# Performance work log

Hardware: AMD Instinct MI355X
Metric: run time of the kernel (lower is better)

The kernel has to match this reference:

```python
import jax, jax.numpy as jnp
import numpy as np

B, C, H, W = 16, 256, 64, 64
K = 1024


def setup_inputs() -> dict:
    key = jax.random.key(0)
    k1, k2 = jax.random.split(key)
    z = jax.random.normal(k1, (B, C, H, W), dtype=jnp.float32)
    codebook = jax.random.normal(k2, (K, C), dtype=jnp.float32)
    return {"z": z, "codebook": codebook}


def reference(z, codebook):
    # assign: nearest-code indices via squared euclidean distance
    b, c, h, w = z.shape
    zf = jnp.transpose(z, (0, 2, 3, 1)).reshape(-1, c)            # [N, C]
    # ||z||^2 - 2 z.cb^T + ||cb||^2  -> [N, K]
    dists = (jnp.sum(zf * zf, axis=1, keepdims=True)
             - 2.0 * jnp.einsum('nc,kc->nk', zf, codebook)
             + jnp.sum(codebook * codebook, axis=1)[None, :])
    idx = jnp.argmin(dists, axis=1)                                # [N]
    indices = idx.reshape(b, 1, h, w)                              # [B,1,H,W]
    # embed_code: gather codebook rows, back to BCHW
    zq = codebook[idx].reshape(b, h, w, c)                         # [B,H,W,C]
    zq = jnp.transpose(zq, (0, 3, 1, 2))                           # [B,C,H,W]
    return zq, indices
```

## Files before the change

### kernel.cpp

```cpp
#include <hip/hip_runtime.h>


#define HWSZ 4096
#define CDIM 256
#define KCODES 1024
#define NPIX 65536
#define ZQ_ELEMS (16 * 256 * 4096)
#define MARGIN 0.75f

#define WS_CBSWZ 0
#define WS_CBN64 524288
#define WS_CBN32 532480
#define WS_CNT   536576
#define WS_LISTS 536592

typedef __attribute__((ext_vector_type(8))) short bf16x8;
typedef __attribute__((ext_vector_type(4))) float f32x4;
typedef __attribute__((ext_vector_type(4))) unsigned short us4;

#define MFMA16(a, b, c) __builtin_amdgcn_mfma_f32_16x16x32_bf16(a, b, c, 0, 0, 0)

__device__ __forceinline__ unsigned short f2bf(float f) {
  unsigned u = __float_as_uint(f);
  unsigned r = u + 0x7FFFu + ((u >> 16) & 1u);
  return (unsigned short)(r >> 16);
}

__device__ __forceinline__ void gload_lds16(const void* g, void* l) {
  __builtin_amdgcn_global_load_lds(
      (const __attribute__((address_space(1))) unsigned int*)g,
      (__attribute__((address_space(3))) unsigned int*)l, 16, 0, 0);
}

__device__ __forceinline__ void ins3(unsigned& k1, unsigned& k2, unsigned& k3,
                                     unsigned k) {
  unsigned nk2, nk3;
  asm("v_med3_u32 %0, %1, %2, %3" : "=v"(nk2) : "v"(k1), "v"(k2), "v"(k));
  asm("v_med3_u32 %0, %1, %2, %3" : "=v"(nk3) : "v"(k2), "v"(k3), "v"(k));
  k1 = k1 < k ? k1 : k;
  k2 = nk2;
  k3 = nk3;
}

__device__ __forceinline__ float keyf(unsigned k) {
  return __uint_as_float(k & 0xFFFFFC00u);
}

__global__ void vq_prep(const float* __restrict__ cb,
                        unsigned short* __restrict__ cbswz,
                        double* __restrict__ cbn64,
                        float* __restrict__ cbn32p,
                        int* __restrict__ cnt) {
  const int t = threadIdx.x;
  if (blockIdx.x == 0 && t == 0) { cnt[0] = 0; cnt[1] = 0; }
  const int code = blockIdx.x * 4 + (t >> 6);
  const int lane = t & 63;
  const int c4 = lane * 4;

  float4 v = *(const float4*)(cb + (size_t)code * CDIM + c4);
  us4 hv;
  hv.x = f2bf(-2.f * v.x); hv.y = f2bf(-2.f * v.y);
  hv.z = f2bf(-2.f * v.z); hv.w = f2bf(-2.f * v.w);
  const int K = (code >> 9) * 32 + ((code >> 4) & 31);
  unsigned r = (unsigned)(code & 15);
  unsigned off = ((r << 9) + (unsigned)(c4 << 1)) ^ ((r & 7) << 4);
  *(us4*)((char*)cbswz + (size_t)K * 8192 + off) = hv;

  double s = (double)v.x * v.x;
  s = fma((double)v.y, (double)v.y, s);
  s = fma((double)v.z, (double)v.z, s);
  s = fma((double)v.w, (double)v.w, s);
#pragma unroll
  for (int o = 32; o; o >>= 1) s += __shfl_xor(s, o, 64);
  if (lane == 0) {
    cbn64[code] = s;
    cbn32p[code] = (float)s + 512.0f;
  }
}

__launch_bounds__(256)
__global__ void vq_stage1(const float* __restrict__ z,
                          const float* __restrict__ cb,
                          const unsigned short* __restrict__ cbswz,
                          const float* __restrict__ cbn32p,
                          float* __restrict__ out_zq,
                          float* __restrict__ out_idx,
                          int* __restrict__ cnt,
                          int* __restrict__ listA, int capA,
                          int* __restrict__ listB, int capB,
                          float* __restrict__ zws, int zcap) {
  extern __shared__ char smem[];
  const int t = threadIdx.x;
  const int w = t >> 6;
  const int lane = t & 63;
  const int lg = lane >> 4;
  const int lcode = lane & 15;
  const int h = w >> 1;
  const int q = w & 1;
  const int p0 = blockIdx.x * 64;
  const int b = p0 >> 12;
  const int hw0 = p0 & (HWSZ - 1);
  const float* zb = z + (size_t)b * (CDIM * HWSZ) + hw0;

  float* nrm = (float*)(smem + 32768);
  {
    float4 nv = *(const float4*)(cbn32p + t * 4);
    *(float4*)(nrm + t * 4) = nv;
  }

  {
    const char* gsrc = (const char*)cbswz + (size_t)(q * 32) * 8192 +
                       (h * 4) * 1024 + lane * 16;
    char* ldst = smem + q * 8192 + (h * 4) * 1024 + lane * 16;
#pragma unroll
    for (int j = 0; j < 4; ++j)
      gload_lds16(gsrc + j * 1024, ldst + j * 1024);
  }

  bf16x8 af[2][8];
#pragma unroll
  for (int T = 0; T < 2; ++T) {
    const float* zr = zb + (h * 32 + T * 16 + lcode);
#pragma unroll
    for (int kk = 0; kk < 8; ++kk) {
      const int ch0 = kk * 32 + lg * 8;
      bf16x8 f;
#pragma unroll
      for (int j = 0; j < 8; ++j)
        f[j] = (short)f2bf(zr[(size_t)(ch0 + j) * HWSZ]);
      af[T][kk] = f;
    }
  }
  __syncthreads();

  unsigned k1[2][4], k2[2][4], k3[2][4];
#pragma unroll
  for (int T = 0; T < 2; ++T)
#pragma unroll
    for (int q4 = 0; q4 < 4; ++q4) {
      k1[T][q4] = 0xFFFFFFFFu; k2[T][q4] = 0xFFFFFFFFu; k3[T][q4] = 0xFFFFFFFFu;
    }

  const unsigned rsw = ((unsigned)(lcode & 7)) << 4;
  const unsigned rbase = ((unsigned)lcode << 9) + (((unsigned)lg) << 4);
  const char* myhalf = smem + q * 8192;
  const int nrm0 = q * 512 + lcode;

  for (int c = 0; c < 32; ++c) {
    const char* rbuf = myhalf + (c & 1) * 16384;
    if (c < 31) {
      const char* gsrc = (const char*)cbswz + (size_t)(q * 32 + c + 1) * 8192 +
                         (h * 4) * 1024 + lane * 16;
      char* ldst = smem + ((c + 1) & 1) * 16384 + q * 8192 +
                   (h * 4) * 1024 + lane * 16;
#pragma unroll
      for (int j = 0; j < 4; ++j)
        gload_lds16(gsrc + j * 1024, ldst + j * 1024);
    }
    f32x4 acc0 = {0.f, 0.f, 0.f, 0.f};
    f32x4 acc1 = {0.f, 0.f, 0.f, 0.f};
#pragma unroll
    for (int kk = 0; kk < 8; ++kk) {
      bf16x8 bf = *(const bf16x8*)(rbuf + ((rbase + ((unsigned)kk << 6)) ^ rsw));
      acc0 = MFMA16(af[0][kk], bf, acc0);
      acc1 = MFMA16(af[1][kk], bf, acc1);
    }
    const unsigned code = (unsigned)(nrm0 + c * 16);
    const float cn = nrm[code];
#pragma unroll
    for (int T = 0; T < 2; ++T)
#pragma unroll
      for (int q4 = 0; q4 < 4; ++q4) {
        float m = cn + ((T == 0) ? acc0[q4] : acc1[q4]);
        unsigned key = (__float_as_uint(m) & 0xFFFFFC00u) | code;
        ins3(k1[T][q4], k2[T][q4], k3[T][q4], key);
      }
    __syncthreads();
  }

#pragma unroll
  for (int mask = 1; mask <= 8; mask <<= 1) {
#pragma unroll
    for (int T = 0; T < 2; ++T)
#pragma unroll
      for (int q4 = 0; q4 < 4; ++q4) {
        unsigned o1 = __shfl_xor(k1[T][q4], mask, 64);
        unsigned o2 = __shfl_xor(k2[T][q4], mask, 64);
        unsigned o3 = __shfl_xor(k3[T][q4], mask, 64);
        ins3(k1[T][q4], k2[T][q4], k3[T][q4], o1);
        ins3(k1[T][q4], k2[T][q4], k3[T][q4], o2);
        ins3(k1[T][q4], k2[T][q4], k3[T][q4], o3);
      }
  }

  unsigned* mk = (unsigned*)smem;
  int* lcnt = (int*)(smem + 2304);
  if (t == 0) *lcnt = 0;
  if (lcode == 0) {
#pragma unroll
    for (int T = 0; T < 2; ++T)
#pragma unroll
      for (int q4 = 0; q4 < 4; ++q4) {
        int row = h * 32 + T * 16 + lg * 4 + q4;
        unsigned* d = mk + (row * 2 + q) * 3;
        d[0] = k1[T][q4]; d[1] = k2[T][q4]; d[2] = k3[T][q4];
      }
  }
  __syncthreads();

  int* sbest = (int*)(smem + 2048);
  int* flp = (int*)(smem + 2560);
  int* flq = (int*)(smem + 2816);
  if (t < 64) {
    unsigned a1 = mk[t * 6 + 0], a2 = mk[t * 6 + 1], a3 = mk[t * 6 + 2];
    ins3(a1, a2, a3, mk[t * 6 + 3]);
    ins3(a1, a2, a3, mk[t * 6 + 4]);
    ins3(a1, a2, a3, mk[t * 6 + 5]);
    const int p = p0 + t;
    const int i1 = (int)(a1 & 1023u);
    sbest[t] = i1;
    out_idx[p] = (float)i1;
    float f1 = keyf(a1);
    float g2 = keyf(a2) - f1;
    float g3 = keyf(a3) - f1;
    if (g3 < MARGIN) {
      int pos = atomicAdd(cnt + 1, 1);
      if (pos < capB) listB[pos] = p;
    } else if (g2 < MARGIN) {
      int pos = atomicAdd(cnt, 1);
      if (pos < capA) {
        listA[2 * pos] = p | (i1 << 16);
        listA[2 * pos + 1] = (int)(a2 & 1023u) | ((int)(a3 & 1023u) << 16);
        if (pos < zcap) {
          int li = atomicAdd(lcnt, 1);
          flp[li] = p;
          flq[li] = pos;
        }
      }
    }
  }
  __syncthreads();

  {
    const int px = t & 63;
    const int best = sbest[px];
    const int ch0g = (t >> 6) * 64;
    const float* crow = cb + (size_t)best * CDIM + ch0g;
    float* ob = out_zq + (size_t)b * (CDIM * HWSZ) + (size_t)ch0g * HWSZ + hw0 + px;
#pragma unroll 4
    for (int c2 = 0; c2 < 64; c2 += 4) {
      float4 v = *(const float4*)(crow + c2);
      ob[(size_t)(c2 + 0) * HWSZ] = v.x;
      ob[(size_t)(c2 + 1) * HWSZ] = v.y;
      ob[(size_t)(c2 + 2) * HWSZ] = v.z;
      ob[(size_t)(c2 + 3) * HWSZ] = v.w;
    }
  }

  {
    const int nf = *lcnt;
    for (int e = 0; e < nf; ++e) {
      const int p = flp[e];
      const int slot = flq[e];
      const int bb = p >> 12;
      const int hh = p & (HWSZ - 1);
      zws[(size_t)slot * 256 + t] =
          z[(size_t)bb * (CDIM * HWSZ) + (size_t)t * HWSZ + hh];
    }
  }
}

__launch_bounds__(256)
__global__ void vq_resolve3(const float* __restrict__ z,
                            const float* __restrict__ cb,
                            const double* __restrict__ cbn64,
                            float* __restrict__ out_zq,
                            float* __restrict__ out_idx,
                            const int* __restrict__ cnt,
                            const int* __restrict__ listA, int capA,
                            const float* __restrict__ zws, int zcap) {
  const int lane = threadIdx.x & 63;
  const int wid = (blockIdx.x * blockDim.x + threadIdx.x) >> 6;
  const int nw = (gridDim.x * blockDim.x) >> 6;
  int n = cnt[0];
  if (n > capA) n = capA;

  for (int i = wid; i < n; i += nw) {
    const int e0 = listA[2 * i];
    const int e1 = listA[2 * i + 1];
    const int p = e0 & 0xFFFF;
    int cand[3];
    cand[0] = (e0 >> 16) & 1023;
    cand[1] = e1 & 0xFFFF;
    cand[2] = (e1 >> 16) & 1023;
    const int b = p >> 12;
    const int hw = p & (HWSZ - 1);
    const int ch0 = lane * 4;

    double zv[4];
    if (i < zcap) {
      float4 zf = ((const float4*)(zws + (size_t)i * 256))[lane];
      zv[0] = (double)zf.x; zv[1] = (double)zf.y;
      zv[2] = (double)zf.z; zv[3] = (double)zf.w;
    } else {
      const float* zb = z + (size_t)b * (CDIM * HWSZ) + hw;
#pragma unroll
      for (int j = 0; j < 4; ++j) zv[j] = (double)zb[(size_t)(ch0 + j) * HWSZ];
    }

    double d[3];
#pragma unroll
    for (int tt = 0; tt < 3; ++tt) {
      float4 cv = *(const float4*)(cb + (size_t)cand[tt] * CDIM + ch0);
      double s = zv[0] * (double)cv.x;
      s = fma(zv[1], (double)cv.y, s);
      s = fma(zv[2], (double)cv.z, s);
      s = fma(zv[3], (double)cv.w, s);
#pragma unroll
      for (int off = 32; off; off >>= 1) s += __shfl_xor(s, off, 64);
      d[tt] = fma(-2.0, s, cbn64[cand[tt]]);
    }

    double bd = d[0];
    int bi = cand[0];
#pragma unroll
    for (int tt = 1; tt < 3; ++tt) {
      bool takes = (d[tt] < bd) || (d[tt] == bd && cand[tt] < bi);
      bd = takes ? d[tt] : bd;
      bi = takes ? cand[tt] : bi;
    }

    if (bi != cand[0]) {
      if (lane == 0) out_idx[p] = (float)bi;
      float4 cv = *(const float4*)(cb + (size_t)bi * CDIM + ch0);
      float* ob = out_zq + (size_t)b * (CDIM * HWSZ) + hw;
      ob[(size_t)(ch0 + 0) * HWSZ] = cv.x;
      ob[(size_t)(ch0 + 1) * HWSZ] = cv.y;
      ob[(size_t)(ch0 + 2) * HWSZ] = cv.z;
      ob[(size_t)(ch0 + 3) * HWSZ] = cv.w;
    }
  }
}

__launch_bounds__(256)
__global__ void vq_fullscan(const float* __restrict__ z,
                            const float* __restrict__ cb,
                            const double* __restrict__ cbn64,
                            float* __restrict__ out_zq,
                            float* __restrict__ out_idx,
                            const int* __restrict__ cnt,
                            const int* __restrict__ listB, int capB) {
  __shared__ double zl[256];
  __shared__ double sd[4];
  __shared__ int si[4];
  __shared__ int sfin;
  int n = cnt[1];
  if (n > capB) n = capB;
  const int t = threadIdx.x;
  const int w = t >> 6;
  const int lane = t & 63;

  for (int i = blockIdx.x; i < n; i += gridDim.x) {
    const int p = listB[i];
    const int b = p >> 12;
    const int hw = p & (HWSZ - 1);
    const float* zb = z + (size_t)b * (CDIM * HWSZ) + hw;
    zl[t] = (double)zb[(size_t)t * HWSZ];
    __syncthreads();

    const int g = t >> 2;
    const int sub = t & 3;
    const double* zq4 = zl + sub * 64;
    double bd = 1e300;
    int bi = 0;

    for (int j = 0; j < 16; ++j) {
      const int code = g + 64 * j;
      const float* crow = cb + (size_t)code * CDIM + sub * 64;
      double s = 0.0;
#pragma unroll
      for (int q4 = 0; q4 < 64; q4 += 4) {
        float4 cv = *(const float4*)(crow + q4);
        s = fma(zq4[q4 + 0], (double)cv.x, s);
        s = fma(zq4[q4 + 1], (double)cv.y, s);
        s = fma(zq4[q4 + 2], (double)cv.z, s);
        s = fma(zq4[q4 + 3], (double)cv.w, s);
      }
      s += __shfl_xor(s, 1, 64);
      s += __shfl_xor(s, 2, 64);
      double d = fma(-2.0, s, cbn64[code]);
      bool takes = (d < bd) || (d == bd && code < bi);
      bd = takes ? d : bd;
      bi = takes ? code : bi;
    }

#pragma unroll
    for (int off = 4; off <= 32; off <<= 1) {
      double od = __shfl_xor(bd, off, 64);
      int oi = __shfl_xor(bi, off, 64);
      bool takes = (od < bd) || (od == bd && oi < bi);
      bd = takes ? od : bd;
      bi = takes ? oi : bi;
    }
    if (lane == 0) { sd[w] = bd; si[w] = bi; }
    __syncthreads();
    if (t == 0) {
      double fd = sd[0];
      int fi = si[0];
#pragma unroll
      for (int k = 1; k < 4; ++k) {
        bool takes = (sd[k] < fd) || (sd[k] == fd && si[k] < fi);
        fd = takes ? sd[k] : fd;
        fi = takes ? si[k] : fi;
      }
      const int old = (int)out_idx[p];
      if (fi != old) out_idx[p] = (float)fi;
      sfin = (fi != old) ? fi : -1;
    }
    __syncthreads();
    const int best = sfin;
    if (best >= 0) {
      float* ob = out_zq + (size_t)b * (CDIM * HWSZ) + hw;
      ob[(size_t)t * HWSZ] = cb[(size_t)best * CDIM + t];
    }
    __syncthreads();
  }
}

extern "C" void kernel_launch(void* const* d_in, const int* in_sizes, int n_in,
                              void* d_out, int out_size, void* d_ws, size_t ws_size,
                              hipStream_t stream) {
  const float* z = (const float*)d_in[0];
  const float* cb = (const float*)d_in[1];
  float* out = (float*)d_out;
  float* out_zq = out;
  float* out_idx = out + ZQ_ELEMS;

  char* ws = (char*)d_ws;
  unsigned short* cbswz = (unsigned short*)(ws + WS_CBSWZ);
  double* cbn64 = (double*)(ws + WS_CBN64);
  float* cbn32p = (float*)(ws + WS_CBN32);
  int* cnt = (int*)(ws + WS_CNT);

  long long avail = (long long)ws_size - WS_LISTS;
  if (avail < 0) avail = 0;
  long long capA_ll = (avail / 4) / 8;
  if (capA_ll > NPIX) capA_ll = NPIX;
  int capA = (int)capA_ll;
  int* listA = (int*)(ws + WS_LISTS);
  long long rem = avail - (long long)capA * 8;
  long long capB_ll = rem / 8;
  if (capB_ll > NPIX) capB_ll = NPIX;
  if (capB_ll < 0) capB_ll = 0;
  int capB = (int)capB_ll;
  int* listB = (int*)(ws + WS_LISTS + (size_t)capA * 8);
  long long zoff = (WS_LISTS + (long long)capA * 8 + (long long)capB * 4 + 15) &
                   ~15LL;
  long long zcap_ll = ((long long)ws_size - zoff) / 1024;
  if (zcap_ll < 0) zcap_ll = 0;
  if (zcap_ll > capA) zcap_ll = capA;
  int zcap = (int)zcap_ll;
  float* zws = (float*)(ws + zoff);

  vq_prep<<<256, 256, 0, stream>>>(cb, cbswz, cbn64, cbn32p, cnt);
  vq_stage1<<<1024, 256, 36864, stream>>>(z, cb, cbswz, cbn32p, out_zq, out_idx,
                                          cnt, listA, capA, listB, capB,
                                          zws, zcap);
  vq_resolve3<<<1024, 256, 0, stream>>>(z, cb, cbn64, out_zq, out_idx,
                                        cnt, listA, capA, zws, zcap);
  vq_fullscan<<<256, 256, 0, stream>>>(z, cb, cbn64, out_zq, out_idx,
                                       cnt, listB, capB);
}
```

Baseline: 164.0 us.

## Triple-buffer codebook staging in stage1 with explicit waitcnt barriers

Replaces the double-buffered codebook LDS pipeline in the stage1 kernel with a three-buffer rotation that prefetches two chunks ahead. Each step now uses a manual vmcnt wait plus a raw barrier instead of __syncthreads. The codebook layout changes from an XOR-swizzled row layout to a kk-major layout, which makes the LDS read addresses simpler. LDS per block grows from 36 KB to 52 KB, which may lower occupancy, and the new unswizzled layout may bring back bank conflicts.

```diff
diff --git a/kernel.cpp b/kernel.cpp
--- a/kernel.cpp
+++ b/kernel.cpp
@@ -62,9 +62,11 @@
   hv.x = f2bf(-2.f * v.x); hv.y = f2bf(-2.f * v.y);
   hv.z = f2bf(-2.f * v.z); hv.w = f2bf(-2.f * v.w);
   const int K = (code >> 9) * 32 + ((code >> 4) & 31);
-  unsigned r = (unsigned)(code & 15);
-  unsigned off = ((r << 9) + (unsigned)(c4 << 1)) ^ ((r & 7) << 4);
-  *(us4*)((char*)cbswz + (size_t)K * 8192 + off) = hv;
+  const int kk = c4 >> 5;
+  const int lg = (c4 >> 3) & 3;
+  const int within = (c4 & 7) * 2;
+  size_t off = (size_t)K * 8192 + kk * 1024 + (code & 15) * 64 + lg * 16 + within;
+  *(us4*)((char*)cbswz + off) = hv;
 
   double s = (double)v.x * v.x;
   s = fma((double)v.y, (double)v.y, s);
@@ -102,20 +104,27 @@
   const int hw0 = p0 & (HWSZ - 1);
   const float* zb = z + (size_t)b * (CDIM * HWSZ) + hw0;
 
-  float* nrm = (float*)(smem + 32768);
-  {
-    float4 nv = *(const float4*)(cbn32p + t * 4);
-    *(float4*)(nrm + t * 4) = nv;
-  }
-
-  {
-    const char* gsrc = (const char*)cbswz + (size_t)(q * 32) * 8192 +
-                       (h * 4) * 1024 + lane * 16;
-    char* ldst = smem + q * 8192 + (h * 4) * 1024 + lane * 16;
-#pragma unroll
-    for (int j = 0; j < 4; ++j)
-      gload_lds16(gsrc + j * 1024, ldst + j * 1024);
-  }
+  char* const bb0 = smem + q * 8192;
+  char* const bb1 = smem + 16384 + q * 8192;
+  char* const bb2 = smem + 32768 + q * 8192;
+  float* nrm = (float*)(smem + 49152);
+  char* scratch = smem + 49152;
+
+  const int stl = h * 4096 + lane * 16;
+  const char* cbbase = (const char*)cbswz + (size_t)q * 262144 + stl;
+
+#define STAGE(CIDX, SBUF)                                             \
+  {                                                                   \
+    const char* gs_ = cbbase + ((size_t)(CIDX) << 13);                \
+    char* ld_ = (SBUF) + stl;                                         \
+    gload_lds16(gs_, ld_);                                            \
+    gload_lds16(gs_ + 1024, ld_ + 1024);                              \
+    gload_lds16(gs_ + 2048, ld_ + 2048);                              \
+    gload_lds16(gs_ + 3072, ld_ + 3072);                              \
+  }
+
+  STAGE(0, bb0);
+  STAGE(1, bb1);
 
   bf16x8 af[2][8];
 #pragma unroll
@@ -131,6 +140,8 @@
       af[T][kk] = f;
     }
   }
+
+  *(float4*)(nrm + t * 4) = *(const float4*)(cbn32p + t * 4);
   __syncthreads();
 
   unsigned k1[2][4], k2[2][4], k3[2][4];
@@ -141,42 +152,48 @@
       k1[T][q4] = 0xFFFFFFFFu; k2[T][q4] = 0xFFFFFFFFu; k3[T][q4] = 0xFFFFFFFFu;
     }
 
-  const unsigned rsw = ((unsigned)(lcode & 7)) << 4;
-  const unsigned rbase = ((unsigned)lcode << 9) + (((unsigned)lg) << 4);
-  const char* myhalf = smem + q * 8192;
-  const int nrm0 = q * 512 + lcode;
-
-  for (int c = 0; c < 32; ++c) {
-    const char* rbuf = myhalf + (c & 1) * 16384;
-    if (c < 31) {
-      const char* gsrc = (const char*)cbswz + (size_t)(q * 32 + c + 1) * 8192 +
-                         (h * 4) * 1024 + lane * 16;
-      char* ldst = smem + ((c + 1) & 1) * 16384 + q * 8192 +
-                   (h * 4) * 1024 + lane * 16;
-#pragma unroll
-      for (int j = 0; j < 4; ++j)
-        gload_lds16(gsrc + j * 1024, ldst + j * 1024);
-    }
-    f32x4 acc0 = {0.f, 0.f, 0.f, 0.f};
-    f32x4 acc1 = {0.f, 0.f, 0.f, 0.f};
-#pragma unroll
-    for (int kk = 0; kk < 8; ++kk) {
-      bf16x8 bf = *(const bf16x8*)(rbuf + ((rbase + ((unsigned)kk << 6)) ^ rsw));
-      acc0 = MFMA16(af[0][kk], bf, acc0);
-      acc1 = MFMA16(af[1][kk], bf, acc1);
-    }
-    const unsigned code = (unsigned)(nrm0 + c * 16);
-    const float cn = nrm[code];
-#pragma unroll
-    for (int T = 0; T < 2; ++T)
-#pragma unroll
-      for (int q4 = 0; q4 < 4; ++q4) {
-        float m = cn + ((T == 0) ? acc0[q4] : acc1[q4]);
-        unsigned key = (__float_as_uint(m) & 0xFFFFFC00u) | code;
-        ins3(k1[T][q4], k2[T][q4], k3[T][q4], key);
-      }
-    __syncthreads();
-  }
+  const int bq = lcode * 64 + lg * 16;
+  const float* nrmp = nrm + q * 512 + lcode;
+  const int kbase = q * 512 + lcode;
+
+#define BODY(CIDX, RBUF, SBUF, DOSTAGE, WN)                           \
+  {                                                                   \
+    asm volatile("s_waitcnt vmcnt(" WN ")" ::: "memory");             \
+    __builtin_amdgcn_s_barrier();                                     \
+    __builtin_amdgcn_sched_barrier(0);                                \
+    if (DOSTAGE) STAGE((CIDX) + 2, SBUF);                             \
+    const char* pb_ = (RBUF) + bq;                                    \
+    f32x4 acc0 = {0.f, 0.f, 0.f, 0.f};                                \
+    f32x4 acc1 = {0.f, 0.f, 0.f, 0.f};                                \
+    _Pragma("unroll")                                                 \
+    for (int kk = 0; kk < 8; ++kk) {                                  \
+      bf16x8 bf_ = *(const bf16x8*)(pb_ + kk * 1024);                 \
+      acc0 = MFMA16(af[0][kk], bf_, acc0);                            \
+      acc1 = MFMA16(af[1][kk], bf_, acc1);                            \
+    }                                                                 \
+    const unsigned code_ = (unsigned)(kbase + (CIDX) * 16);           \
+    const float cn_ = nrmp[(CIDX) * 16];                              \
+    _Pragma("unroll")                                                 \
+    for (int q4 = 0; q4 < 4; ++q4) {                                  \
+      float m0_ = cn_ + acc0[q4];                                     \
+      ins3(k1[0][q4], k2[0][q4], k3[0][q4],                           \
+           (__float_as_uint(m0_) & 0xFFFFFC00u) | code_);             \
+      float m1_ = cn_ + acc1[q4];                                     \
+      ins3(k1[1][q4], k2[1][q4], k3[1][q4],                           \
+           (__float_as_uint(m1_) & 0xFFFFFC00u) | code_);             \
+    }                                                                 \
+  }
+
+#pragma unroll 1
+  for (int c3 = 0; c3 < 30; c3 += 3) {
+    BODY(c3 + 0, bb0, bb2, 1, "4");
+    BODY(c3 + 1, bb1, bb0, 1, "4");
+    BODY(c3 + 2, bb2, bb1, 1, "4");
+  }
+  BODY(30, bb0, bb2, 0, "4");
+  BODY(31, bb1, bb0, 0, "0");
+#undef BODY
+#undef STAGE
 
 #pragma unroll
   for (int mask = 1; mask <= 8; mask <<= 1) {
@@ -193,8 +210,11 @@
       }
   }
 
-  unsigned* mk = (unsigned*)smem;
-  int* lcnt = (int*)(smem + 2304);
+  unsigned* mk = (unsigned*)scratch;
+  int* sbest = (int*)(scratch + 1536);
+  int* flp = (int*)(scratch + 1792);
+  int* flq = (int*)(scratch + 2048);
+  int* lcnt = (int*)(scratch + 2304);
   if (t == 0) *lcnt = 0;
   if (lcode == 0) {
 #pragma unroll
@@ -208,9 +228,6 @@
   }
   __syncthreads();
 
-  int* sbest = (int*)(smem + 2048);
-  int* flp = (int*)(smem + 2560);
-  int* flq = (int*)(smem + 2816);
   if (t < 64) {
     unsigned a1 = mk[t * 6 + 0], a2 = mk[t * 6 + 1], a3 = mk[t * 6 + 2];
     ins3(a1, a2, a3, mk[t * 6 + 3]);
@@ -414,8 +431,8 @@
         fi = takes ? si[k] : fi;
       }
       const int old = (int)out_idx[p];
+      sfin = (fi != old) ? fi : -1;
       if (fi != old) out_idx[p] = (float)fi;
-      sfin = (fi != old) ? fi : -1;
     }
     __syncthreads();
     const int best = sfin;
@@ -463,7 +480,7 @@
   float* zws = (float*)(ws + zoff);
 
   vq_prep<<<256, 256, 0, stream>>>(cb, cbswz, cbn64, cbn32p, cnt);
-  vq_stage1<<<1024, 256, 36864, stream>>>(z, cb, cbswz, cbn32p, out_zq, out_idx,
+  vq_stage1<<<1024, 256, 53248, stream>>>(z, cb, cbswz, cbn32p, out_zq, out_idx,
                                           cnt, listA, capA, listB, capB,
                                           zws, zcap);
   vq_resolve3<<<1024, 256, 0, stream>>>(z, cb, cbn64, out_zq, out_idx,
```

Result: faster. 155.6 us (-5.2%).
